# Optimization experiments

Measured on AMD Instinct MI355X. Metric: run time of the kernel, lower is better.

Reference implementation:

```python
import jax, jax.numpy as jnp
import numpy as np

SATURATION = 1.0


def setup_inputs() -> dict:
    key = jax.random.key(0)
    k1, k2, k3, k4, k5 = jax.random.split(key, 5)
    B, Q, C = 128, 2048, 8
    L, K = 256, 64
    ts = jax.random.normal(k1, (B, Q, C), dtype=jnp.float32)
    shapelets = jax.random.normal(k2, (L, K, C), dtype=jnp.float32)  # stacked ParameterList
    gating = jax.random.normal(k3, (L,), dtype=jnp.float32)
    fc1_w = jax.random.normal(k4, (2, L), dtype=jnp.float32) / np.sqrt(L)
    fc1_b = jax.random.normal(k5, (2,), dtype=jnp.float32) * 0.01
    return {"ts": ts, "shapelets": shapelets, "gating": gating,
            "fc1_w": fc1_w, "fc1_b": fc1_b}


def reference(ts, shapelets, gating, fc1_w, fc1_b):
    # ts: [B, Q, C]; shapelets: [L, K, C]
    ts = ts.astype(jnp.float32)
    L, K, C = shapelets.shape
    # ||segment||^2 summed over (K, C) via sliding-window cumsum trick -> [B, S]
    ts2 = jnp.sum(ts * ts, axis=2)                     # [B, Q]
    csum = jnp.pad(jnp.cumsum(ts2, axis=1), ((0, 0), (1, 0)))
    win_sq = csum[:, K:] - csum[:, :-K]                # [B, S], S = Q-K+1
    # cross term <segment, shapelet> for all windows/shapelets via 1D conv
    kernel = jnp.transpose(shapelets, (1, 2, 0))       # [K, C, L] (WIO)
    cross = jax.lax.conv_general_dilated(
        ts, kernel, window_strides=(1,), padding='VALID',
        dimension_numbers=('NWC', 'WIO', 'NWC'))       # [B, S, L]
    sh_sq = jnp.sum(shapelets * shapelets, axis=(1, 2))  # [L]
    # mean squared distance per (batch, window, shapelet)
    dist = (win_sq[:, :, None] - 2.0 * cross + sh_sq[None, None, :]) / (K * C)
    hard_min = jnp.min(dist, axis=1)                   # [B, L] min-pool over windows
    g = jax.nn.sigmoid(SATURATION * gating)            # [L]
    min_dw = hard_min * g                              # equivalent to result @ diag(g)
    return min_dw @ fc1_w.T + fc1_b                    # [B, 2]
```

## Files before the change

kernel.cpp:

```cpp
#include <hip/hip_runtime.h>
#include <stdint.h>

#define B_ 128
#define Q_ 2048
#define C_ 8
#define L_ 256
#define K_ 64
#define S_ 1985
#define KC_ 512

typedef short s16x8 __attribute__((ext_vector_type(8)));
typedef float f32x16 __attribute__((ext_vector_type(16)));

__device__ __forceinline__ unsigned short f2bf(float f) {
    unsigned u = __float_as_uint(f);
    u += 0x7FFFu + ((u >> 16) & 1u);
    return (unsigned short)(u >> 16);
}
__device__ __forceinline__ unsigned fenc(float f) {
    unsigned u = __float_as_uint(f);
    return (u & 0x80000000u) ? ~u : (u | 0x80000000u);
}
__device__ __forceinline__ float fdec(unsigned k) {
    unsigned u = (k & 0x80000000u) ? (k ^ 0x80000000u) : ~k;
    return __uint_as_float(u);
}
__device__ __forceinline__ void async_copy16(void* lds_dst, const void* g_src) {
    __builtin_amdgcn_global_load_lds(
        (const __attribute__((address_space(1))) void*)g_src,
        (__attribute__((address_space(3))) void*)lds_dst, 16, 0, 0);
}

__global__ __launch_bounds__(256) void k_prep(const float* __restrict__ ts,
                                              const float* __restrict__ sh,
                                              uint4* __restrict__ tsb,
                                              uint4* __restrict__ shb2,
                                              float* __restrict__ shsq,
                                              unsigned* __restrict__ extg,
                                              unsigned* __restrict__ hmin) {
    __shared__ float t2[2048];
    const int bid = blockIdx.x, t = threadIdx.x;
    if (bid < 128) {
        const int b = bid;
        #pragma unroll
        for (int j = 0; j < 8; ++j) {
            int r = j * 256 + t;
            const float4* p = (const float4*)(ts + ((size_t)b * Q_ + r) * C_);
            float4 x = p[0], y = p[1];
            union { unsigned short h[8]; uint4 v; } u;
            u.h[0] = f2bf(x.x); u.h[1] = f2bf(x.y); u.h[2] = f2bf(x.z); u.h[3] = f2bf(x.w);
            u.h[4] = f2bf(y.x); u.h[5] = f2bf(y.y); u.h[6] = f2bf(y.z); u.h[7] = f2bf(y.w);
            tsb[(size_t)b * Q_ + r] = u.v;
            t2[r] = x.x*x.x + x.y*x.y + x.z*x.z + x.w*x.w
                  + y.x*y.x + y.y*y.y + y.z*y.z + y.w*y.w;
        }
        __syncthreads();
        int s0 = t * 8;
        float w = 0.f;
        if (s0 < S_) {
            #pragma unroll 16
            for (int k = 0; k < K_; ++k) w += t2[s0 + k];
        }
        #pragma unroll
        for (int j = 0; j < 8; ++j) {
            int s = s0 + j;
            unsigned word = 0x0000FF80u;
            if (s < S_) {
                float v = -0.5f * w;
                unsigned short hh = f2bf(v);
                float hf = __uint_as_float((unsigned)hh << 16);
                unsigned short ll = f2bf(v - hf);
                word = (unsigned)hh | ((unsigned)ll << 16);
            }
            extg[(size_t)b * Q_ + s] = word;
            if (s + K_ < Q_) w += t2[s + K_] - t2[s];
        }
    } else if (bid < 192) {
        const int l = (bid - 128) * 4 + (t >> 6);
        const int c = t & 63;
        const float4* p = (const float4*)(sh + (size_t)l * KC_) + c * 2;
        float4 x = p[0], y = p[1];
        union { unsigned short h[8]; uint4 v; } u;
        u.h[0] = f2bf(x.x); u.h[1] = f2bf(x.y); u.h[2] = f2bf(x.z); u.h[3] = f2bf(x.w);
        u.h[4] = f2bf(y.x); u.h[5] = f2bf(y.y); u.h[6] = f2bf(y.z); u.h[7] = f2bf(y.w);
        shb2[c * L_ + l] = u.v;
        float ss = x.x*x.x + x.y*x.y + x.z*x.z + x.w*x.w
                 + y.x*y.x + y.y*y.y + y.z*y.z + y.w*y.w;
        #pragma unroll
        for (int off = 32; off >= 1; off >>= 1) ss += __shfl_down(ss, off, 64);
        if (c == 0) shsq[l] = ss;
    } else if (bid < 194) {
        uint4 z; z.x = z.y = z.z = z.w = 0u;
        tsb[B_ * Q_ + (bid - 192) * 256 + t] = z;
    } else {
        hmin[(bid - 194) * 256 + t] = 0xFFFFFFFFu;
    }
}

__global__ __launch_bounds__(256, 3) void k_main(
    const uint4* __restrict__ tsb,
    const uint4* __restrict__ shb2,
    const unsigned* __restrict__ extg,
    const float* __restrict__ shsq,
    unsigned*    __restrict__ hmin)
{
    __shared__ uint4 a_lds[192];

    const int ms   = blockIdx.x >> 1;
    const int nt   = blockIdx.x & 1;
    const int b    = blockIdx.y;
    const int m0   = ms * 512;
    const int c0   = nt * 128;
    const int tid  = threadIdx.x;
    const int lane = tid & 63;
    const int wv   = tid >> 6;
    const int l31  = lane & 31;
    const int hi   = lane >> 5;
    const int wm   = wv >> 1;
    const int wn   = wv & 1;

    #define STAGE_A(mi_)                                                       \
        if (tid < 192)                                                         \
            async_copy16((char*)a_lds + tid * 16,                              \
                         (const char*)(tsb + (size_t)b * Q_ + m0 + (mi_) * 128)\
                         + tid * 16);

    const f32x16 fz = {0.f,0.f,0.f,0.f,0.f,0.f,0.f,0.f,
                       0.f,0.f,0.f,0.f,0.f,0.f,0.f,0.f};
    const float inf = __builtin_inff();
    float rm0 = inf, rm1 = inf;

    const char* ab    = (const char*)a_lds;
    const int   arow  = wm * 64 + l31 + hi;
    const char* bbase = (const char*)shb2 + (size_t)(c0 + wn * 64 + l31) * 16;

    union UU { unsigned u[4]; s16x8 v; };
    UU be; be.u[0] = hi ? 0u : 0x3F803F80u;
    be.u[1] = 0u; be.u[2] = 0u; be.u[3] = 0u;

    #pragma unroll 1
    for (int mi = 0; mi < 4; ++mi) {
        STAGE_A(mi)
        size_t eb = (size_t)b * Q_ + m0 + mi * 128 + wm * 64 + l31;
        unsigned w0 = extg[eb];
        unsigned w1 = extg[eb + 32];
        __syncthreads();

        f32x16 acc00 = fz, acc01 = fz;
        f32x16 acc10 = fz, acc11 = fz;
        #pragma unroll 4
        for (int kk = 0; kk < 32; ++kk) {
            s16x8 a0 = *(const s16x8*)(ab + (arow + 2 * kk) * 16);
            s16x8 a1 = *(const s16x8*)(ab + (arow + 2 * kk) * 16 + 512);
            const char* bp = bbase + (size_t)(2 * kk + hi) * 4096;
            s16x8 b0 = *(const s16x8*)(bp);
            s16x8 b1 = *(const s16x8*)(bp + 512);
            __builtin_amdgcn_s_setprio(1);
            acc00 = __builtin_amdgcn_mfma_f32_32x32x16_bf16(a0, b0, acc00, 0, 0, 0);
            acc01 = __builtin_amdgcn_mfma_f32_32x32x16_bf16(a0, b1, acc01, 0, 0, 0);
            acc10 = __builtin_amdgcn_mfma_f32_32x32x16_bf16(a1, b0, acc10, 0, 0, 0);
            acc11 = __builtin_amdgcn_mfma_f32_32x32x16_bf16(a1, b1, acc11, 0, 0, 0);
            __builtin_amdgcn_s_setprio(0);
        }
        {
            UU ae0, ae1;
            ae0.u[0] = hi ? 0u : w0; ae0.u[1] = 0; ae0.u[2] = 0; ae0.u[3] = 0;
            ae1.u[0] = hi ? 0u : w1; ae1.u[1] = 0; ae1.u[2] = 0; ae1.u[3] = 0;
            acc00 = __builtin_amdgcn_mfma_f32_32x32x16_bf16(ae0.v, be.v, acc00, 0, 0, 0);
            acc01 = __builtin_amdgcn_mfma_f32_32x32x16_bf16(ae0.v, be.v, acc01, 0, 0, 0);
            acc10 = __builtin_amdgcn_mfma_f32_32x32x16_bf16(ae1.v, be.v, acc10, 0, 0, 0);
            acc11 = __builtin_amdgcn_mfma_f32_32x32x16_bf16(ae1.v, be.v, acc11, 0, 0, 0);
        }
        #pragma unroll
        for (int r = 0; r < 16; ++r) {
            rm0 = fminf(rm0, fminf(-2.f * acc00[r], -2.f * acc10[r]));
            rm1 = fminf(rm1, fminf(-2.f * acc01[r], -2.f * acc11[r]));
        }
        __syncthreads();
    }

    const int colg = c0 + wn * 64 + l31;
    rm0 = (rm0 + shsq[colg])      * (1.f / 512.f);
    rm1 = (rm1 + shsq[colg + 32]) * (1.f / 512.f);
    rm0 = fminf(rm0, __shfl_xor(rm0, 32, 64));
    rm1 = fminf(rm1, __shfl_xor(rm1, 32, 64));
    if (hi == 0) {
        atomicMin(&hmin[b * L_ + colg],      fenc(rm0));
        atomicMin(&hmin[b * L_ + colg + 32], fenc(rm1));
    }
}

__global__ __launch_bounds__(256) void k_final(const unsigned* __restrict__ hmin,
                                               const float* __restrict__ gating,
                                               const float* __restrict__ w,
                                               const float* __restrict__ bias,
                                               float* __restrict__ out) {
    const int b = blockIdx.x, t = threadIdx.x;
    float v = fdec(hmin[b * L_ + t]);
    float g = 1.f / (1.f + __expf(-gating[t]));
    float mg = v * g;
    float p0 = mg * w[t];
    float p1 = mg * w[L_ + t];
    #pragma unroll
    for (int off = 32; off >= 1; off >>= 1) {
        p0 += __shfl_down(p0, off, 64);
        p1 += __shfl_down(p1, off, 64);
    }
    __shared__ float r0[4], r1[4];
    int wvi = t >> 6, ln = t & 63;
    if (ln == 0) { r0[wvi] = p0; r1[wvi] = p1; }
    __syncthreads();
    if (t == 0) {
        out[b * 2 + 0] = r0[0] + r0[1] + r0[2] + r0[3] + bias[0];
        out[b * 2 + 1] = r1[0] + r1[1] + r1[2] + r1[3] + bias[1];
    }
}

extern "C" void kernel_launch(void* const* d_in, const int* in_sizes, int n_in,
                              void* d_out, int out_size, void* d_ws, size_t ws_size,
                              hipStream_t stream) {
    const float* ts     = (const float*)d_in[0];
    const float* sh     = (const float*)d_in[1];
    const float* gating = (const float*)d_in[2];
    const float* fw     = (const float*)d_in[3];
    const float* fb     = (const float*)d_in[4];
    float* out = (float*)d_out;

    char* ws = (char*)d_ws;
    uint4*    tsb  = (uint4*)ws;
    uint4*    shb2 = (uint4*)(ws + 4202496);
    float*    shsq = (float*)(ws + 4464640);
    unsigned* hmin = (unsigned*)(ws + 4465664);
    unsigned* extg = (unsigned*)(ws + 4596736);

    k_prep<<<322, 256, 0, stream>>>(ts, sh, tsb, shb2, shsq, extg, hmin);
    dim3 grid(8, B_);
    k_main<<<grid, 256, 0, stream>>>(tsb, shb2, extg, shsq, hmin);
    k_final<<<128, 256, 0, stream>>>(hmin, gating, fw, fb, out);
}
```

Baseline: 77.54 us.

## Stage shapelet tiles in double-buffered LDS and widen per-wave tile to 96 rows

The main kernel now covers 192 windows per block in a single pass. Each wave holds six 32x32 accumulators, a 3x2 tile, instead of four. Shapelet operand chunks are copied asynchronously into a double-buffered LDS area and overlapped with the MFMA loop, instead of being read straight from global memory on every window sub-tile. The tail rows of the last tile reuse a clamped norm index. This is meant to cut repeated global/L2 traffic for the B operand and raise MFMA work per load. The costs are more blocks, a few extra padded rows of work, more accumulator registers and a barrier per K chunk.

Measured after the change: 71.98 us. -7.2%, faster.

```diff
diff --git a/kernel.cpp b/kernel.cpp
--- a/kernel.cpp
+++ b/kernel.cpp
@@ -8,6 +8,7 @@
 #define K_ 64
 #define S_ 1985
 #define KC_ 512
+#define MT_ 11
 
 typedef short s16x8 __attribute__((ext_vector_type(8)));
 typedef float f32x16 __attribute__((ext_vector_type(16)));
@@ -104,12 +105,13 @@
     const float* __restrict__ shsq,
     unsigned*    __restrict__ hmin)
 {
-    __shared__ uint4 a_lds[192];
-
-    const int ms   = blockIdx.x >> 1;
+    __shared__ uint4 b_lds[2][1024];
+    __shared__ uint4 a_lds[256];
+
+    const int mt   = blockIdx.x >> 1;
     const int nt   = blockIdx.x & 1;
     const int b    = blockIdx.y;
-    const int m0   = ms * 512;
+    const int r0   = mt * 192;
     const int c0   = nt * 128;
     const int tid  = threadIdx.x;
     const int lane = tid & 63;
@@ -119,64 +121,88 @@
     const int wm   = wv >> 1;
     const int wn   = wv & 1;
 
-    #define STAGE_A(mi_)                                                       \
-        if (tid < 192)                                                         \
-            async_copy16((char*)a_lds + tid * 16,                              \
-                         (const char*)(tsb + (size_t)b * Q_ + m0 + (mi_) * 128)\
-                         + tid * 16);
+    #define STAGE_B(p, buf)                                                    \
+        {                                                                      \
+            _Pragma("unroll")                                                  \
+            for (int i = 0; i < 4; ++i) {                                      \
+                int e  = i * 256 + tid;                           \
+                int ch = e >> 7, col = e & 127;                                \
+                async_copy16((char*)&b_lds[buf][e],                            \
+                             (const char*)(shb2 + ((p) * 8 + ch) * L_ + c0 + col)); \
+            }                                                                  \
+        }
+
+    async_copy16((char*)a_lds + tid * 16,
+                 (const char*)(tsb + (size_t)b * Q_ + r0) + tid * 16);
+    STAGE_B(0, 0)
+    __syncthreads();
 
     const f32x16 fz = {0.f,0.f,0.f,0.f,0.f,0.f,0.f,0.f,
                        0.f,0.f,0.f,0.f,0.f,0.f,0.f,0.f};
-    const float inf = __builtin_inff();
-    float rm0 = inf, rm1 = inf;
+    f32x16 acc00 = fz, acc01 = fz;
+    f32x16 acc10 = fz, acc11 = fz;
+    f32x16 acc20 = fz, acc21 = fz;
 
     const char* ab    = (const char*)a_lds;
-    const int   arow  = wm * 64 + l31 + hi;
-    const char* bbase = (const char*)shb2 + (size_t)(c0 + wn * 64 + l31) * 16;
-
-    union UU { unsigned u[4]; s16x8 v; };
-    UU be; be.u[0] = hi ? 0u : 0x3F803F80u;
-    be.u[1] = 0u; be.u[2] = 0u; be.u[3] = 0u;
+    const int   arow  = wm * 96 + l31 + hi;
+    const int   bcolb = (wn * 64 + l31) * 16;
 
     #pragma unroll 1
-    for (int mi = 0; mi < 4; ++mi) {
-        STAGE_A(mi)
-        size_t eb = (size_t)b * Q_ + m0 + mi * 128 + wm * 64 + l31;
-        unsigned w0 = extg[eb];
-        unsigned w1 = extg[eb + 32];
-        __syncthreads();
-
-        f32x16 acc00 = fz, acc01 = fz;
-        f32x16 acc10 = fz, acc11 = fz;
-        #pragma unroll 4
-        for (int kk = 0; kk < 32; ++kk) {
-            s16x8 a0 = *(const s16x8*)(ab + (arow + 2 * kk) * 16);
-            s16x8 a1 = *(const s16x8*)(ab + (arow + 2 * kk) * 16 + 512);
-            const char* bp = bbase + (size_t)(2 * kk + hi) * 4096;
-            s16x8 b0 = *(const s16x8*)(bp);
-            s16x8 b1 = *(const s16x8*)(bp + 512);
+    for (int p = 0; p < 8; ++p) {
+        if (p < 7) STAGE_B(p + 1, (p + 1) & 1)
+        const char* bb = (const char*)&b_lds[p & 1][0];
+        #pragma unroll
+        for (int kkl = 0; kkl < 4; ++kkl) {
+            int rb = arow + 2 * (p * 4 + kkl);
+            s16x8 a0 = *(const s16x8*)(ab + rb * 16);
+            s16x8 a1 = *(const s16x8*)(ab + rb * 16 + 512);
+            s16x8 a2 = *(const s16x8*)(ab + rb * 16 + 1024);
+            int ch = 2 * kkl + hi;
+            s16x8 b0 = *(const s16x8*)(bb + ch * 2048 + bcolb);
+            s16x8 b1 = *(const s16x8*)(bb + ch * 2048 + bcolb + 512);
             __builtin_amdgcn_s_setprio(1);
             acc00 = __builtin_amdgcn_mfma_f32_32x32x16_bf16(a0, b0, acc00, 0, 0, 0);
             acc01 = __builtin_amdgcn_mfma_f32_32x32x16_bf16(a0, b1, acc01, 0, 0, 0);
             acc10 = __builtin_amdgcn_mfma_f32_32x32x16_bf16(a1, b0, acc10, 0, 0, 0);
             acc11 = __builtin_amdgcn_mfma_f32_32x32x16_bf16(a1, b1, acc11, 0, 0, 0);
+            acc20 = __builtin_amdgcn_mfma_f32_32x32x16_bf16(a2, b0, acc20, 0, 0, 0);
+            acc21 = __builtin_amdgcn_mfma_f32_32x32x16_bf16(a2, b1, acc21, 0, 0, 0);
             __builtin_amdgcn_s_setprio(0);
         }
-        {
-            UU ae0, ae1;
-            ae0.u[0] = hi ? 0u : w0; ae0.u[1] = 0; ae0.u[2] = 0; ae0.u[3] = 0;
-            ae1.u[0] = hi ? 0u : w1; ae1.u[1] = 0; ae1.u[2] = 0; ae1.u[3] = 0;
-            acc00 = __builtin_amdgcn_mfma_f32_32x32x16_bf16(ae0.v, be.v, acc00, 0, 0, 0);
-            acc01 = __builtin_amdgcn_mfma_f32_32x32x16_bf16(ae0.v, be.v, acc01, 0, 0, 0);
-            acc10 = __builtin_amdgcn_mfma_f32_32x32x16_bf16(ae1.v, be.v, acc10, 0, 0, 0);
-            acc11 = __builtin_amdgcn_mfma_f32_32x32x16_bf16(ae1.v, be.v, acc11, 0, 0, 0);
-        }
-        #pragma unroll
-        for (int r = 0; r < 16; ++r) {
-            rm0 = fminf(rm0, fminf(-2.f * acc00[r], -2.f * acc10[r]));
-            rm1 = fminf(rm1, fminf(-2.f * acc01[r], -2.f * acc11[r]));
-        }
         __syncthreads();
+    }
+
+    union UU { unsigned u[4]; s16x8 v; };
+    UU be; be.u[0] = hi ? 0u : 0x3F803F80u;
+    be.u[1] = 0u; be.u[2] = 0u; be.u[3] = 0u;
+    {
+        int rg = r0 + wm * 96 + l31;
+        int e0 = rg      > 2047 ? 2047 : rg;
+        int e1 = rg + 32 > 2047 ? 2047 : rg + 32;
+        int e2 = rg + 64 > 2047 ? 2047 : rg + 64;
+        unsigned w0 = extg[(size_t)b * Q_ + e0];
+        unsigned w1 = extg[(size_t)b * Q_ + e1];
+        unsigned w2 = extg[(size_t)b * Q_ + e2];
+        UU a0, a1, a2;
+        a0.u[0] = hi ? 0u : w0; a0.u[1] = 0; a0.u[2] = 0; a0.u[3] = 0;
+        a1.u[0] = hi ? 0u : w1; a1.u[1] = 0; a1.u[2] = 0; a1.u[3] = 0;
+        a2.u[0] = hi ? 0u : w2; a2.u[1] = 0; a2.u[2] = 0; a2.u[3] = 0;
+        acc00 = __builtin_amdgcn_mfma_f32_32x32x16_bf16(a0.v, be.v, acc00, 0, 0, 0);
+        acc01 = __builtin_amdgcn_mfma_f32_32x32x16_bf16(a0.v, be.v, acc01, 0, 0, 0);
+        acc10 = __builtin_amdgcn_mfma_f32_32x32x16_bf16(a1.v, be.v, acc10, 0, 0, 0);
+        acc11 = __builtin_amdgcn_mfma_f32_32x32x16_bf16(a1.v, be.v, acc11, 0, 0, 0);
+        acc20 = __builtin_amdgcn_mfma_f32_32x32x16_bf16(a2.v, be.v, acc20, 0, 0, 0);
+        acc21 = __builtin_amdgcn_mfma_f32_32x32x16_bf16(a2.v, be.v, acc21, 0, 0, 0);
+    }
+
+    const float inf = __builtin_inff();
+    float rm0 = inf, rm1 = inf;
+    #pragma unroll
+    for (int r = 0; r < 16; ++r) {
+        rm0 = fminf(rm0, fminf(-2.f * acc00[r],
+                    fminf(-2.f * acc10[r], -2.f * acc20[r])));
+        rm1 = fminf(rm1, fminf(-2.f * acc01[r],
+                    fminf(-2.f * acc11[r], -2.f * acc21[r])));
     }
 
     const int colg = c0 + wn * 64 + l31;
@@ -234,7 +260,7 @@
     unsigned* extg = (unsigned*)(ws + 4596736);
 
     k_prep<<<322, 256, 0, stream>>>(ts, sh, tsb, shb2, shsq, extg, hmin);
-    dim3 grid(8, B_);
+    dim3 grid(MT_ * 2, B_);
     k_main<<<grid, 256, 0, stream>>>(tsb, shb2, extg, shsq, hmin);
     k_final<<<128, 256, 0, stream>>>(hmin, gating, fw, fb, out);
 }
```
